# Performance work log

Measured on AMD Instinct MI355X. Metric: run time of the kernel, lower is better.

The kernel has to match this reference:

```python
import jax, jax.numpy as jnp
import numpy as np

MAX_SOURCE_LEN = 2048
HIDDEN = 1024
HEADS = 16
NUM_BUCKETS = 32
MAX_DISTANCE = 128
LN_EPS = 1e-5


def relative_position_bucket(relative_position, num_buckets=NUM_BUCKETS, max_distance=MAX_DISTANCE):
    # Bidirectional T5-style bucketing.
    n = -relative_position
    half = num_buckets // 2
    ret = (n < 0).astype(jnp.int32) * half
    n = jnp.abs(n)
    max_exact = half // 2
    is_small = n < max_exact
    scale = (half - max_exact) / np.log(max_distance / max_exact)
    val_large = max_exact + (jnp.log(jnp.maximum(n, 1).astype(jnp.float32) / max_exact) * scale).astype(jnp.int32)
    val_large = jnp.minimum(val_large, half - 1)
    return ret + jnp.where(is_small, n.astype(jnp.int32), val_large)


def setup_inputs() -> dict:
    key = jax.random.key(0)
    ks = jax.random.split(key, 6)
    B, L = 4, 1024
    leaf_idx = jax.random.randint(ks[0], (B, L), 0, MAX_SOURCE_LEN)
    p_emb = jax.random.normal(ks[1], (MAX_SOURCE_LEN, HIDDEN), jnp.float32) * 0.02
    p_emb = p_emb.at[0].set(0.0)  # padding_idx=0
    r_emb = jax.random.normal(ks[2], (NUM_BUCKETS + 1, HEADS), jnp.float32) * 0.02
    r_emb = r_emb.at[NUM_BUCKETS].set(0.0)  # padding_idx=num_buckets
    Wq = jax.random.normal(ks[3], (HIDDEN, HIDDEN), jnp.float32) / np.sqrt(HIDDEN)
    Wk = jax.random.normal(ks[4], (HIDDEN, HIDDEN), jnp.float32) / np.sqrt(HIDDEN)
    return {
        "leaf_idx": leaf_idx,
        "p_emb": p_emb,
        "r_emb": r_emb,
        "ln_g": jnp.ones((HIDDEN,), jnp.float32),
        "ln_b": jnp.zeros((HIDDEN,), jnp.float32),
        "Wq": Wq,
        "bq": jnp.zeros((HIDDEN,), jnp.float32),
        "Wk": Wk,
        "bk": jnp.zeros((HIDDEN,), jnp.float32),
    }


def reference(leaf_idx, p_emb, r_emb, ln_g, ln_b, Wq, bq, Wk, bk):
    B, L = leaf_idx.shape
    H = r_emb.shape[1]
    d_k = p_emb.shape[1] // H

    # --- T5 relative-position bias ---
    # rel[b,i,j] = leaf[b,j] - leaf[b,i]  (matches unsqueeze(1) - unsqueeze(-1))
    rel = leaf_idx[:, None, :] - leaf_idx[:, :, None]
    bucket = relative_position_bucket(rel)
    valid = leaf_idx != 0
    pair = valid[:, None, :] & valid[:, :, None]
    bucket = jnp.where(pair, bucket, NUM_BUCKETS)
    t5_score = jnp.transpose(r_emb[bucket], (0, 3, 1, 2))  # [B,H,L,L]

    # --- untied position score ---
    x = p_emb[leaf_idx]  # [B,L,D]
    mu = jnp.mean(x, axis=-1, keepdims=True)
    var = jnp.mean(jnp.square(x - mu), axis=-1, keepdims=True)
    xn = (x - mu) * jax.lax.rsqrt(var + LN_EPS) * ln_g + ln_b

    q = (xn @ Wq.T + bq).reshape(B, L, H, d_k).transpose(0, 2, 1, 3) / np.sqrt(d_k)
    k = (xn @ Wk.T + bk).reshape(B, L, H, d_k).transpose(0, 2, 1, 3)
    untied = jnp.einsum("bhid,bhjd->bhij", q, k)

    return untied + t5_score  # leaf_PE_Type == 'Merge'
```

## Files before the change

kernel.cpp:

```cpp
#include <hip/hip_runtime.h>
#include <hip/hip_bf16.h>

typedef __attribute__((ext_vector_type(8))) short short8;
typedef __attribute__((ext_vector_type(4))) float f32x4;

#define L 1024
#define D 1024
#define NHEADS 16

static __device__ __forceinline__ unsigned short f2bf(float f) {
  union { float f; unsigned int u; } c; c.f = f;
  unsigned int u = c.u;
  u += 0x7fffu + ((u >> 16) & 1u);
  return (unsigned short)(u >> 16);
}

static __device__ __forceinline__ void gload_lds16(const void* gsrc, void* ldst) {
  __builtin_amdgcn_global_load_lds(
      (const __attribute__((address_space(1))) void*)gsrc,
      (__attribute__((address_space(3))) void*)ldst, 16, 0, 0);
}

__global__ __launch_bounds__(256) void prep_kernel(const int* __restrict__ leaf,
                                                   const float* __restrict__ p_emb,
                                                   const float* __restrict__ g,
                                                   const float* __restrict__ bcoef,
                                                   const float* __restrict__ Wq,
                                                   const float* __restrict__ Wk,
                                                   unsigned short* __restrict__ w,
                                                   unsigned short* __restrict__ xn,
                                                   unsigned char* __restrict__ bucket) {
  int bid = blockIdx.x;
  int t = threadIdx.x;
  if (bid < 2048) {
    int idx = bid * 256 + t;
    const float* src = (idx < 262144) ? Wq : Wk;
    int rel = (idx < 262144) ? idx : idx - 262144;
    float4 v = ((const float4*)src)[rel];
    ushort4 o;
    o.x = f2bf(v.x); o.y = f2bf(v.y); o.z = f2bf(v.z); o.w = f2bf(v.w);
    ((ushort4*)w)[idx] = o;
  } else if (bid < 6144) {
    int row = bid - 2048;
    int lane = t & 63, wv = t >> 6;
    int leafv = leaf[row];
    float4 xv = ((const float4*)(p_emb + (size_t)leafv * D))[t];
    float s  = xv.x + xv.y + xv.z + xv.w;
    float s2 = xv.x*xv.x + xv.y*xv.y + xv.z*xv.z + xv.w*xv.w;
    #pragma unroll
    for (int o = 1; o < 64; o <<= 1) {
      s  += __shfl_xor(s, o);
      s2 += __shfl_xor(s2, o);
    }
    __shared__ float red[8];
    if (lane == 0) { red[wv*2] = s; red[wv*2+1] = s2; }
    __syncthreads();
    float st  = red[0] + red[2] + red[4] + red[6];
    float s2t = red[1] + red[3] + red[5] + red[7];
    float mu = st * (1.0f/1024.0f);
    float var = s2t * (1.0f/1024.0f) - mu*mu;
    float rs = rsqrtf(var + 1e-5f);
    float4 gv = ((const float4*)g)[t];
    float4 bv = ((const float4*)bcoef)[t];
    ushort4 o;
    o.x = f2bf((xv.x - mu) * rs * gv.x + bv.x);
    o.y = f2bf((xv.y - mu) * rs * gv.y + bv.y);
    o.z = f2bf((xv.z - mu) * rs * gv.z + bv.z);
    o.w = f2bf((xv.w - mu) * rs * gv.w + bv.w);
    ((ushort4*)xn)[row * 256 + t] = o;
  } else {
    int idx = (bid - 6144) * 256 + t;
    int j = idx & 1023;
    int rest = idx >> 10;
    int i = rest & 1023;
    int b = rest >> 10;
    int li = leaf[b * L + i];
    int lj = leaf[b * L + j];
    int n = li - lj;
    int ret = 0;
    if (n < 0) { ret = 16; n = -n; }
    int val;
    if (n < 8) {
      val = n;
    } else {
      val = 8 + (int)(logf((float)n * 0.125f) * 2.8853900817779268f);
      if (val > 15) val = 15;
    }
    val += ret;
    if (li == 0 || lj == 0) val = 32;
    bucket[idx] = (unsigned char)val;
  }
}

__global__ __launch_bounds__(256) void qk_gemm_kernel(const unsigned short* __restrict__ xn,
                                                      const unsigned short* __restrict__ wqk,
                                                      const float* __restrict__ bq,
                                                      const float* __restrict__ bk,
                                                      unsigned short* __restrict__ qws,
                                                      unsigned short* __restrict__ kws) {
  __shared__ __align__(16) unsigned short As[2][128 * 32];
  __shared__ __align__(16) unsigned short Bs[2][128 * 32];
  int t = threadIdx.x;
  int lane = t & 63, w = t >> 6;
  int wr = w >> 1, wc = w & 1;
  int wg = blockIdx.x;
  int swz = (wg & 7) * 64 + (wg >> 3);
  int m0 = (swz >> 4) * 128;
  int n0 = (swz & 15) * 128;

  f32x4 acc[4][4] = {};

  auto stage = [&](int buf, int kt) {
    int k0 = kt * 32;
    #pragma unroll
    for (int r = 0; r < 2; ++r) {
      int c = t + r * 256;
      int row = c >> 2, kc = c & 3;
      gload_lds16(xn  + (size_t)(m0 + row) * D + k0 + kc * 8, &As[buf][c * 8]);
      gload_lds16(wqk + (size_t)(n0 + row) * D + k0 + kc * 8, &Bs[buf][c * 8]);
    }
  };

  stage(0, 0);
  __syncthreads();
  for (int kt = 0; kt < 32; ++kt) {
    int cur = kt & 1;
    if (kt < 31) stage(cur ^ 1, kt + 1);
    short8 a[4], b[4];
    #pragma unroll
    for (int f = 0; f < 4; ++f) {
      int arow = wr * 64 + f * 16 + (lane & 15);
      a[f] = *(const short8*)&As[cur][arow * 32 + (lane >> 4) * 8];
      int brow = wc * 64 + f * 16 + (lane & 15);
      b[f] = *(const short8*)&Bs[cur][brow * 32 + (lane >> 4) * 8];
    }
    #pragma unroll
    for (int i = 0; i < 4; ++i)
      #pragma unroll
      for (int j = 0; j < 4; ++j)
        acc[i][j] = __builtin_amdgcn_mfma_f32_16x16x32_bf16(b[j], a[i], acc[i][j], 0, 0, 0);
    __syncthreads();
  }

  bool isq = (n0 < 1024);
  const float* bias = isq ? bq : bk;
  float scale = isq ? 0.125f : 1.0f;
  unsigned short* outp = isq ? qws : kws;
  int nbase = n0 - (isq ? 0 : 1024);

  float4 bv[4];
  #pragma unroll
  for (int j = 0; j < 4; ++j)
    bv[j] = *(const float4*)(bias + nbase + wc * 64 + j * 16 + (lane >> 4) * 4);

  #pragma unroll
  for (int i = 0; i < 4; ++i) {
    int m = m0 + wr * 64 + i * 16 + (lane & 15);
    int bb = m >> 10, ii = m & 1023;
    #pragma unroll
    for (int j = 0; j < 4; ++j) {
      int n0c = nbase + wc * 64 + j * 16 + (lane >> 4) * 4;
      int h = n0c >> 6, k0 = n0c & 63;
      int bh = bb * NHEADS + h;
      float v0 = (acc[i][j][0] + bv[j].x) * scale;
      float v1 = (acc[i][j][1] + bv[j].y) * scale;
      float v2 = (acc[i][j][2] + bv[j].z) * scale;
      float v3 = (acc[i][j][3] + bv[j].w) * scale;
      unsigned p0 = (unsigned)f2bf(v0) | ((unsigned)f2bf(v1) << 16);
      unsigned p1 = (unsigned)f2bf(v2) | ((unsigned)f2bf(v3) << 16);
      size_t off = (size_t)bh * 65536 + (size_t)(ii >> 4) * 1024
                 + (size_t)(k0 >> 3) * 128 + (ii & 15) * 8 + (k0 & 7);
      uint2 pv; pv.x = p0; pv.y = p1;
      *(uint2*)(outp + off) = pv;
    }
  }
}

__global__ __launch_bounds__(256) void untied_kernel(const unsigned short* __restrict__ qws,
                                                     const unsigned short* __restrict__ kws,
                                                     const unsigned char* __restrict__ bucket,
                                                     const float* __restrict__ r_emb,
                                                     float* __restrict__ out) {
  __shared__ float rt[33 * 17];
  __shared__ __align__(16) unsigned char bt[128 * 128];
  int t = threadIdx.x;
  for (int idx = t; idx < 528; idx += 256)
    rt[(idx >> 4) * 17 + (idx & 15)] = r_emb[idx];

  int bid = blockIdx.x;
  int lg = (bid & 7) * 512 + (bid >> 3);
  int h  = lg & 15;
  int jt = (lg >> 4) & 7;
  int it = (lg >> 7) & 7;
  int b  = lg >> 10;
  int lane = t & 63, w = t >> 6;
  int wr = w >> 1, wc = w & 1;
  int i0 = it * 128, j0 = jt * 128;
  int bh = b * NHEADS + h;

  const unsigned char* bsrc = bucket + (size_t)b * L * L + (size_t)i0 * L + j0;
  {
    #pragma unroll
    for (int iter = 0; iter < 4; ++iter) {
      int lofs = iter * 4096 + w * 1024 + lane * 16;
      int row = lofs >> 7;
      int cb = (lofs >> 4) & 7;
      gload_lds16(bsrc + (size_t)row * L + (size_t)((cb ^ (row & 7)) << 4), &bt[lofs]);
    }
  }

  const unsigned short* qb = qws + (size_t)bh * 65536;
  const unsigned short* kb = kws + (size_t)bh * 65536;

  short8 a[4][2], bf[4][2];
  #pragma unroll
  for (int f = 0; f < 4; ++f) {
    #pragma unroll
    for (int ks = 0; ks < 2; ++ks) {
      a[f][ks]  = *(const short8*)(qb + (size_t)(i0 / 16 + wr * 4 + f) * 1024 + ks * 512 + lane * 8);
      bf[f][ks] = *(const short8*)(kb + (size_t)(j0 / 16 + wc * 4 + f) * 1024 + ks * 512 + lane * 8);
    }
  }

  __syncthreads();

  f32x4 acc[4][4] = {};
  #pragma unroll
  for (int ks = 0; ks < 2; ++ks)
    #pragma unroll
    for (int i = 0; i < 4; ++i)
      #pragma unroll
      for (int j = 0; j < 4; ++j)
        acc[i][j] = __builtin_amdgcn_mfma_f32_16x16x32_bf16(bf[j][ks], a[i][ks], acc[i][j], 0, 0, 0);

  float* ob = out + (size_t)bh * L * L;
  const float* rth = rt + h;
  #pragma unroll
  for (int i = 0; i < 4; ++i) {
    int il = wr * 64 + i * 16 + (lane & 15);
    #pragma unroll
    for (int j = 0; j < 4; ++j) {
      int jl = wc * 64 + j * 16 + (lane >> 4) * 4;
      int jd = jl >> 2;
      int addr = il * 128 + (((jd >> 2) ^ (il & 7)) << 4) + ((jd & 3) << 2);
      unsigned bw = *(const unsigned*)&bt[addr];
      float4 o;
      o.x = acc[i][j][0] + rth[(bw & 255u) * 17];
      o.y = acc[i][j][1] + rth[((bw >> 8) & 255u) * 17];
      o.z = acc[i][j][2] + rth[((bw >> 16) & 255u) * 17];
      o.w = acc[i][j][3] + rth[(bw >> 24) * 17];
      *(float4*)(ob + (size_t)(i0 + il) * L + (j0 + jl)) = o;
    }
  }
}

extern "C" void kernel_launch(void* const* d_in, const int* in_sizes, int n_in,
                              void* d_out, int out_size, void* d_ws, size_t ws_size,
                              hipStream_t stream) {
  const int*   leaf  = (const int*)d_in[0];
  const float* p_emb = (const float*)d_in[1];
  const float* r_emb = (const float*)d_in[2];
  const float* ln_g  = (const float*)d_in[3];
  const float* ln_b  = (const float*)d_in[4];
  const float* Wq    = (const float*)d_in[5];
  const float* bq    = (const float*)d_in[6];
  const float* Wk    = (const float*)d_in[7];
  const float* bk    = (const float*)d_in[8];
  float* out = (float*)d_out;

  char* ws = (char*)d_ws;
  unsigned short* xn   = (unsigned short*)(ws);
  unsigned short* wqk  = (unsigned short*)(ws + (8u  << 20));
  unsigned short* qws  = (unsigned short*)(ws + (12u << 20));
  unsigned short* kws  = (unsigned short*)(ws + (20u << 20));
  unsigned char*  bckt = (unsigned char*)(ws + (28u << 20));

  prep_kernel<<<22528, 256, 0, stream>>>(leaf, p_emb, ln_g, ln_b, Wq, Wk, wqk, xn, bckt);
  qk_gemm_kernel<<<512, 256, 0, stream>>>(xn, wqk, bq, bk, qws, kws);
  untied_kernel<<<4096, 256, 0, stream>>>(qws, kws, bckt, r_emb, out);
}
```

Before: 108.9 us.

## Halve QK GEMM tile width to double workgroups and fold scale into weights

The Q/K projection GEMM now uses 128x64 tiles instead of 128x128, launching 1024 workgroups instead of 512 so more of the GPU's compute units stay busy. The 1/sqrt(d_k) scale is folded into the bf16 conversion of Wq and into the bias, which removes a per-element multiply from the epilogue. In the untied kernel, all bucket bytes are loaded from LDS before the output adds, so the LDS reads can overlap. Smaller tiles mean less data reuse per workgroup and more global traffic for xn, and scaling before rounding to bf16 changes rounding slightly.

```diff
diff --git a/kernel.cpp b/kernel.cpp
--- a/kernel.cpp
+++ b/kernel.cpp
@@ -34,11 +34,13 @@
   int t = threadIdx.x;
   if (bid < 2048) {
     int idx = bid * 256 + t;
-    const float* src = (idx < 262144) ? Wq : Wk;
-    int rel = (idx < 262144) ? idx : idx - 262144;
+    bool isq = (idx < 262144);
+    const float* src = isq ? Wq : Wk;
+    float sc = isq ? 0.125f : 1.0f;
+    int rel = isq ? idx : idx - 262144;
     float4 v = ((const float4*)src)[rel];
     ushort4 o;
-    o.x = f2bf(v.x); o.y = f2bf(v.y); o.z = f2bf(v.z); o.w = f2bf(v.w);
+    o.x = f2bf(v.x * sc); o.y = f2bf(v.y * sc); o.z = f2bf(v.z * sc); o.w = f2bf(v.w * sc);
     ((ushort4*)w)[idx] = o;
   } else if (bid < 6144) {
     int row = bid - 2048;
@@ -99,16 +101,16 @@
                                                       unsigned short* __restrict__ qws,
                                                       unsigned short* __restrict__ kws) {
   __shared__ __align__(16) unsigned short As[2][128 * 32];
-  __shared__ __align__(16) unsigned short Bs[2][128 * 32];
+  __shared__ __align__(16) unsigned short Bs[2][64 * 32];
   int t = threadIdx.x;
   int lane = t & 63, w = t >> 6;
   int wr = w >> 1, wc = w & 1;
   int wg = blockIdx.x;
-  int swz = (wg & 7) * 64 + (wg >> 3);
-  int m0 = (swz >> 4) * 128;
-  int n0 = (swz & 15) * 128;
-
-  f32x4 acc[4][4] = {};
+  int swz = (wg & 7) * 128 + (wg >> 3);
+  int m0 = (swz >> 5) * 128;
+  int n0 = (swz & 31) * 64;
+
+  f32x4 acc[4][2] = {};
 
   auto stage = [&](int buf, int kt) {
     int k0 = kt * 32;
@@ -116,8 +118,11 @@
     for (int r = 0; r < 2; ++r) {
       int c = t + r * 256;
       int row = c >> 2, kc = c & 3;
-      gload_lds16(xn  + (size_t)(m0 + row) * D + k0 + kc * 8, &As[buf][c * 8]);
-      gload_lds16(wqk + (size_t)(n0 + row) * D + k0 + kc * 8, &Bs[buf][c * 8]);
+      gload_lds16(xn + (size_t)(m0 + row) * D + k0 + kc * 8, &As[buf][c * 8]);
+    }
+    {
+      int row = t >> 2, kc = t & 3;
+      gload_lds16(wqk + (size_t)(n0 + row) * D + k0 + kc * 8, &Bs[buf][t * 8]);
     }
   };
 
@@ -126,18 +131,21 @@
   for (int kt = 0; kt < 32; ++kt) {
     int cur = kt & 1;
     if (kt < 31) stage(cur ^ 1, kt + 1);
-    short8 a[4], b[4];
+    short8 a[4], b[2];
     #pragma unroll
     for (int f = 0; f < 4; ++f) {
       int arow = wr * 64 + f * 16 + (lane & 15);
       a[f] = *(const short8*)&As[cur][arow * 32 + (lane >> 4) * 8];
-      int brow = wc * 64 + f * 16 + (lane & 15);
+    }
+    #pragma unroll
+    for (int f = 0; f < 2; ++f) {
+      int brow = wc * 32 + f * 16 + (lane & 15);
       b[f] = *(const short8*)&Bs[cur][brow * 32 + (lane >> 4) * 8];
     }
     #pragma unroll
     for (int i = 0; i < 4; ++i)
       #pragma unroll
-      for (int j = 0; j < 4; ++j)
+      for (int j = 0; j < 2; ++j)
         acc[i][j] = __builtin_amdgcn_mfma_f32_16x16x32_bf16(b[j], a[i], acc[i][j], 0, 0, 0);
     __syncthreads();
   }
@@ -148,26 +156,24 @@
   unsigned short* outp = isq ? qws : kws;
   int nbase = n0 - (isq ? 0 : 1024);
 
-  float4 bv[4];
-  #pragma unroll
-  for (int j = 0; j < 4; ++j)
-    bv[j] = *(const float4*)(bias + nbase + wc * 64 + j * 16 + (lane >> 4) * 4);
+  float4 bv[2];
+  #pragma unroll
+  for (int j = 0; j < 2; ++j) {
+    bv[j] = *(const float4*)(bias + nbase + wc * 32 + j * 16 + (lane >> 4) * 4);
+    bv[j].x *= scale; bv[j].y *= scale; bv[j].z *= scale; bv[j].w *= scale;
+  }
 
   #pragma unroll
   for (int i = 0; i < 4; ++i) {
     int m = m0 + wr * 64 + i * 16 + (lane & 15);
     int bb = m >> 10, ii = m & 1023;
     #pragma unroll
-    for (int j = 0; j < 4; ++j) {
-      int n0c = nbase + wc * 64 + j * 16 + (lane >> 4) * 4;
+    for (int j = 0; j < 2; ++j) {
+      int n0c = nbase + wc * 32 + j * 16 + (lane >> 4) * 4;
       int h = n0c >> 6, k0 = n0c & 63;
       int bh = bb * NHEADS + h;
-      float v0 = (acc[i][j][0] + bv[j].x) * scale;
-      float v1 = (acc[i][j][1] + bv[j].y) * scale;
-      float v2 = (acc[i][j][2] + bv[j].z) * scale;
-      float v3 = (acc[i][j][3] + bv[j].w) * scale;
-      unsigned p0 = (unsigned)f2bf(v0) | ((unsigned)f2bf(v1) << 16);
-      unsigned p1 = (unsigned)f2bf(v2) | ((unsigned)f2bf(v3) << 16);
+      unsigned p0 = (unsigned)f2bf(acc[i][j][0] + bv[j].x) | ((unsigned)f2bf(acc[i][j][1] + bv[j].y) << 16);
+      unsigned p1 = (unsigned)f2bf(acc[i][j][2] + bv[j].z) | ((unsigned)f2bf(acc[i][j][3] + bv[j].w) << 16);
       size_t off = (size_t)bh * 65536 + (size_t)(ii >> 4) * 1024
                  + (size_t)(k0 >> 3) * 128 + (ii & 15) * 8 + (k0 & 7);
       uint2 pv; pv.x = p0; pv.y = p1;
@@ -233,8 +239,7 @@
       for (int j = 0; j < 4; ++j)
         acc[i][j] = __builtin_amdgcn_mfma_f32_16x16x32_bf16(bf[j][ks], a[i][ks], acc[i][j], 0, 0, 0);
 
-  float* ob = out + (size_t)bh * L * L;
-  const float* rth = rt + h;
+  unsigned bw[4][4];
   #pragma unroll
   for (int i = 0; i < 4; ++i) {
     int il = wr * 64 + i * 16 + (lane & 15);
@@ -243,12 +248,24 @@
       int jl = wc * 64 + j * 16 + (lane >> 4) * 4;
       int jd = jl >> 2;
       int addr = il * 128 + (((jd >> 2) ^ (il & 7)) << 4) + ((jd & 3) << 2);
-      unsigned bw = *(const unsigned*)&bt[addr];
+      bw[i][j] = *(const unsigned*)&bt[addr];
+    }
+  }
+
+  float* ob = out + (size_t)bh * L * L;
+  const float* rth = rt + h;
+  #pragma unroll
+  for (int i = 0; i < 4; ++i) {
+    int il = wr * 64 + i * 16 + (lane & 15);
+    #pragma unroll
+    for (int j = 0; j < 4; ++j) {
+      int jl = wc * 64 + j * 16 + (lane >> 4) * 4;
+      unsigned w32 = bw[i][j];
       float4 o;
-      o.x = acc[i][j][0] + rth[(bw & 255u) * 17];
-      o.y = acc[i][j][1] + rth[((bw >> 8) & 255u) * 17];
-      o.z = acc[i][j][2] + rth[((bw >> 16) & 255u) * 17];
-      o.w = acc[i][j][3] + rth[(bw >> 24) * 17];
+      o.x = acc[i][j][0] + rth[(w32 & 255u) * 17];
+      o.y = acc[i][j][1] + rth[((w32 >> 8) & 255u) * 17];
+      o.z = acc[i][j][2] + rth[((w32 >> 16) & 255u) * 17];
+      o.w = acc[i][j][3] + rth[(w32 >> 24) * 17];
       *(float4*)(ob + (size_t)(i0 + il) * L + (j0 + jl)) = o;
     }
   }
@@ -276,6 +293,6 @@
   unsigned char*  bckt = (unsigned char*)(ws + (28u << 20));
 
   prep_kernel<<<22528, 256, 0, stream>>>(leaf, p_emb, ln_g, ln_b, Wq, Wk, wqk, xn, bckt);
-  qk_gemm_kernel<<<512, 256, 0, stream>>>(xn, wqk, bq, bk, qws, kws);
+  qk_gemm_kernel<<<1024, 256, 0, stream>>>(xn, wqk, bq, bk, qws, kws);
   untied_kernel<<<4096, 256, 0, stream>>>(qws, kws, bckt, r_emb, out);
 }
```

Measured after the change: 105.8 us. -2.9%, faster.
